# Optimization experiments

Hardware: AMD Instinct MI355X
Metric: run time of the kernel (lower is better)

The kernel has to match this reference:

```python
import jax, jax.numpy as jnp
import numpy as np

DIM = 1024
HEADS = 16
HEAD_DIM = DIM // HEADS
N_CLUSTERS = 8
B, N = 4, 1024


def setup_inputs() -> dict:
    key = jax.random.key(0)
    ks = jax.random.split(key, 10)
    s = 0.02
    return {
        "x": jax.random.normal(ks[0], (B, N, DIM), dtype=jnp.float32),
        "Wqkv": jax.random.normal(ks[1], (DIM, 3 * DIM), dtype=jnp.float32) * s,
        "Wproj": jax.random.normal(ks[2], (DIM, DIM), dtype=jnp.float32) * s,
        "bproj": jnp.zeros((DIM,), dtype=jnp.float32),
        "Wgroup": jax.random.normal(ks[3], (HEAD_DIM, N_CLUSTERS), dtype=jnp.float32) * s,
        "bgroup": jnp.zeros((N_CLUSTERS,), dtype=jnp.float32),
        "Wtheta": jax.random.normal(ks[4], (HEAD_DIM, 1), dtype=jnp.float32) * s,
        "btheta": jnp.zeros((1,), dtype=jnp.float32),
        "affinity_B": jax.random.normal(ks[5], (HEADS, N_CLUSTERS, N_CLUSTERS), dtype=jnp.float32),
        "cp_bias_scale": jnp.asarray(1.0, dtype=jnp.float32),
        "flag": 1,
        "injection": 0,
        "cp_dcmm": 1,
    }


def reference(x, Wqkv, Wproj, bproj, Wgroup, bgroup, Wtheta, btheta,
              affinity_B, cp_bias_scale, flag, injection, cp_dcmm):
    b, n, c = x.shape
    h = affinity_B.shape[0]
    hd = c // h
    scale = hd ** -0.5
    # qkv: [b,n,3c] -> [3,b,h,n,hd]
    qkv = (x @ Wqkv).reshape(b, n, 3, h, hd).transpose(2, 0, 3, 1, 4)
    q, k, v = qkv[0], qkv[1], qkv[2]
    attn = jnp.einsum('bhnd,bhmd->bhnm', q, k) * scale
    z_constraint = jnp.asarray(0.0, dtype=x.dtype)
    if cp_dcmm and flag:
        # cluster assignments per query token
        z = jax.nn.softmax(q @ Wgroup + bgroup, axis=-1)          # [b,h,n,K]
        B_aff = jax.nn.sigmoid(affinity_B)                         # [h,K,K]
        zB = jnp.einsum('bhik,hkl->bhil', z, B_aff)
        cp_bias_ori = jnp.tanh(jnp.einsum('bhil,bhjl->bhij', zB, z))  # [b,h,n,n]
        theta = jax.nn.relu(jnp.squeeze(q @ Wtheta + btheta, -1))  # [b,h,n]
        degree_term = theta[..., :, None] * theta[..., None, :]
        cp_bias = cp_bias_scale * degree_term * cp_bias_ori
        attn = attn + cp_bias
        z_constraint = -(z * jnp.log(z + 1e-8)).sum(axis=-1).mean()
    else:
        cp_bias = jnp.zeros_like(attn)
    attn = jax.nn.softmax(attn, axis=-1)
    out = jnp.einsum('bhnm,bhmd->bhnd', attn, v).transpose(0, 2, 1, 3).reshape(b, n, c)
    out = out @ Wproj + bproj
    zero = jnp.asarray(0.0, dtype=x.dtype)
    return (out, z_constraint, zero, zero, cp_bias)
```

## Files before the change

kernel.cpp:

```cpp
#include <hip/hip_runtime.h>
#include <stdint.h>

#define DIM 1024
#define HEADS 16
#define HD 64
#define NC 8
#define BB 4
#define NN 1024
#define ROWS (BB*NN)
#define TOK (BB*HEADS*NN)
#define OUT_OFF_Z (ROWS*DIM)
#define CP_OFF    (ROWS*DIM+3)

typedef __bf16 bf16_t;
typedef __attribute__((ext_vector_type(8))) __bf16 bf16x8;
typedef __attribute__((ext_vector_type(4))) __bf16 bf16x4;
typedef __attribute__((ext_vector_type(4))) float f32x4;

__device__ __forceinline__ void gload16(const void* g, void* l){
#if __has_builtin(__builtin_amdgcn_global_load_lds)
  __builtin_amdgcn_global_load_lds(
      (__attribute__((address_space(1))) void*)(g),
      (__attribute__((address_space(3))) void*)(l), 16, 0, 0);
#else
  *(uint4*)l = *(const uint4*)g;
#endif
}

__device__ __forceinline__ float tanh_poly(float d){
  float t2 = d*d;
  float p = -0.33333333f + t2*(0.13333333f + t2*(-0.05396825f));
  return d*(1.f + t2*p);
}

__global__ __launch_bounds__(256) void prep_kernel(
    const float* __restrict__ x, const float* __restrict__ Wqkv,
    const float* __restrict__ Wproj, const float* __restrict__ affB,
    bf16_t* __restrict__ xb, bf16_t* __restrict__ WqkvT, bf16_t* __restrict__ WprojT,
    float* __restrict__ sigB, float* __restrict__ out_scalars){
  const int bid = blockIdx.x, tid = threadIdx.x;
  if(bid < 4096){
    int i = (bid*256 + tid)*4;
    float4 v = *(const float4*)&x[i];
    bf16x4 o = {(bf16_t)v.x, (bf16_t)v.y, (bf16_t)v.z, (bf16_t)v.w};
    *(bf16x4*)&xb[i] = o;
    return;
  }
  if(bid < 8192){
    __shared__ float tile[32][33];
    const float* in; bf16_t* out; int K, N, bx, by;
    if(bid < 7168){ int t = bid-4096; in = Wqkv;  out = WqkvT;  K = 1024; N = 3072; bx = t%96; by = t/96; }
    else          { int t = bid-7168; in = Wproj; out = WprojT; K = 1024; N = 1024; bx = t%32; by = t/32; }
    int k0 = by*32, n0 = bx*32;
    int tx = tid & 31, ty = tid >> 5;
    #pragma unroll
    for(int r=ty; r<32; r+=8) tile[r][tx] = in[(size_t)(k0+r)*N + n0+tx];
    __syncthreads();
    #pragma unroll
    for(int r=ty; r<32; r+=8) out[(size_t)(n0+r)*K + k0+tx] = (bf16_t)tile[tx][r];
    return;
  }
  #pragma unroll
  for(int r=0;r<4;r++){
    int i = r*256 + tid;
    sigB[i] = 1.f/(1.f + __expf(-affB[i]));
  }
  if(tid < 3) out_scalars[tid] = 0.f;
}

__global__ __launch_bounds__(256) void gemm_qkvt(const bf16_t* __restrict__ xb,
                                                 const bf16_t* __restrict__ WT,
                                                 bf16_t* __restrict__ Qb,
                                                 bf16_t* __restrict__ Kb,
                                                 bf16_t* __restrict__ Vt){
  const int K = DIM;
  __shared__ __align__(16) bf16_t As[128*32];
  __shared__ __align__(16) bf16_t Bs[128*32];
  const int bid = blockIdx.x, tid = threadIdx.x;
  const bool qkmode = bid < 512;
  int m0, n0;
  const bf16_t *Ap, *Bp;
  if(qkmode){ m0 = (bid>>4)*128;            n0 = (bid&15)*128;
              Ap = xb + (size_t)m0*K;       Bp = WT + (size_t)n0*K; }
  else      { int t = bid-512; m0 = (t>>5)*128; n0 = (t&31)*128;
              Ap = WT + (size_t)(2048+m0)*K; Bp = xb + (size_t)n0*K; }
  const int wave = tid>>6, lane = tid&63, l15 = lane&15, quad = lane>>4;
  const int wm = (wave>>1)*64, wn = (wave&1)*64;

  f32x4 acc[4][4];
  #pragma unroll
  for(int i=0;i<4;i++)
    #pragma unroll
    for(int j=0;j<4;j++) acc[i][j] = (f32x4){0.f,0.f,0.f,0.f};

  for(int k0=0; k0<K; k0+=32){
    #pragma unroll
    for(int p=0;p<2;p++){
      int c = tid + p*256;
      int r = c>>2, s = c&3, xs = s ^ ((r>>1)&3);
      gload16(Ap + (size_t)r*K + k0 + xs*8, &As[c*8]);
      gload16(Bp + (size_t)r*K + k0 + xs*8, &Bs[c*8]);
    }
    __syncthreads();

    bf16x8 a[4], b[4];
    #pragma unroll
    for(int i=0;i<4;i++){
      int R = wm + i*16 + l15;
      a[i] = *(const bf16x8*)&As[R*32 + ((quad ^ ((R>>1)&3)))*8];
    }
    #pragma unroll
    for(int j=0;j<4;j++){
      int R = wn + j*16 + l15;
      b[j] = *(const bf16x8*)&Bs[R*32 + ((quad ^ ((R>>1)&3)))*8];
    }
    #pragma unroll
    for(int i=0;i<4;i++)
      #pragma unroll
      for(int j=0;j<4;j++)
        acc[i][j] = __builtin_amdgcn_mfma_f32_16x16x32_bf16(a[i], b[j], acc[i][j], 0,0,0);
    __syncthreads();
  }

  if(qkmode){
    #pragma unroll
    for(int j=0;j<4;j++){
      int col = n0 + wn + j*16 + l15;
      int which = col>>10, hc = col&1023, h = hc>>6, d = hc&63;
      bf16_t* dst = which ? Kb : Qb;
      #pragma unroll
      for(int i=0;i<4;i++){
        int m = m0 + wm + i*16 + quad*4;
        #pragma unroll
        for(int r=0;r<4;r++){
          int row = m + r;
          int bh = (row>>10)*HEADS + h, n = row&1023;
          dst[((size_t)bh*NN + n)*HD + d] = (bf16_t)acc[i][j][r];
        }
      }
    }
  } else {
    const int b = n0 >> 10;
    #pragma unroll
    for(int i=0;i<4;i++)
      #pragma unroll
      for(int j=0;j<4;j++){
        int vcol = m0 + wm + i*16 + quad*4;
        int ncol = (n0 & 1023) + wn + j*16 + l15;
        #pragma unroll
        for(int r=0;r<4;r++)
          Vt[((size_t)(b*1024 + vcol + r))*NN + ncol] = (bf16_t)acc[i][j][r];
      }
  }
}

__global__ __launch_bounds__(256) void token_kernel(
    const bf16_t* __restrict__ Qb, const float* __restrict__ Wgroup,
    const float* __restrict__ bgroup, const float* __restrict__ Wtheta,
    const float* __restrict__ btheta, const float* __restrict__ sigB,
    bf16_t* __restrict__ zb16, bf16_t* __restrict__ zBb16,
    float* __restrict__ thetaAll, float* __restrict__ entPart){
  const int wv = threadIdx.x>>6, lane = threadIdx.x&63;
  const int t = blockIdx.x*4 + wv;
  const int h = (t>>10)&15;
  float qd = (float)Qb[(size_t)t*HD + lane];

  float zl[8];
  #pragma unroll
  for(int c=0;c<8;c++){
    float p = qd * Wgroup[lane*NC + c];
    p += __shfl_xor(p,1);  p += __shfl_xor(p,2);  p += __shfl_xor(p,4);
    p += __shfl_xor(p,8);  p += __shfl_xor(p,16); p += __shfl_xor(p,32);
    zl[c] = p + bgroup[c];
  }
  float th = qd * Wtheta[lane];
  th += __shfl_xor(th,1);  th += __shfl_xor(th,2);  th += __shfl_xor(th,4);
  th += __shfl_xor(th,8);  th += __shfl_xor(th,16); th += __shfl_xor(th,32);
  th = fmaxf(th + btheta[0], 0.f);

  float mx = zl[0];
  #pragma unroll
  for(int c=1;c<8;c++) mx = fmaxf(mx, zl[c]);
  float ssum = 0.f;
  #pragma unroll
  for(int c=0;c<8;c++){ zl[c] = __expf(zl[c]-mx); ssum += zl[c]; }
  float inv = 1.f/ssum;
  float ent = 0.f;
  #pragma unroll
  for(int c=0;c<8;c++){ float z = zl[c]*inv; zl[c] = z; ent -= z*__logf(z + 1e-8f); }

  float zb[8];
  #pragma unroll
  for(int l=0;l<8;l++){
    float a = 0.f;
    #pragma unroll
    for(int k2=0;k2<8;k2++) a += zl[k2]*sigB[h*64 + k2*8 + l];
    zb[l] = a;
  }
  if(lane==0){
    bf16x8 zv, zbv;
    #pragma unroll
    for(int c=0;c<8;c++){ zv[c] = (bf16_t)zl[c]; zbv[c] = (bf16_t)zb[c]; }
    *(bf16x8*)&zb16[(size_t)t*8]  = zv;
    *(bf16x8*)&zBb16[(size_t)t*8] = zbv;
    thetaAll[t] = th;
  }

  __shared__ float es[4];
  if(lane==0) es[wv] = ent;
  __syncthreads();
  if(threadIdx.x==0) entPart[blockIdx.x] = es[0]+es[1]+es[2]+es[3];
}

__global__ __launch_bounds__(256) void bias_kernel(
    const bf16_t* __restrict__ zb16, const bf16_t* __restrict__ zBb16,
    const float* __restrict__ thetaAll, const float* __restrict__ cps_p,
    float* __restrict__ cp_out){
  const int bid = blockIdx.x;
  const int bh = bid & 63, qt = bid >> 6;
  const int tid = threadIdx.x;
  const int wave = tid>>6, lane = tid&63, l15 = lane&15, quad = lane>>4;
  __shared__ float thAll[NN];
  { float4 tv = *(const float4*)&thetaAll[(size_t)bh*NN + tid*4];
    *(float4*)&thAll[tid*4] = tv; }
  const float cps = cps_p[0];
  bf16x8 aZ = (bf16x8)(bf16_t)0.f;
  if(quad==0)
    aZ = *(const bf16x8*)&zBb16[((size_t)bh*NN + qt*64 + wave*16 + l15)*8];
  __syncthreads();
  float th_i[4];
  #pragma unroll
  for(int r=0;r<4;r++) th_i[r] = thAll[qt*64 + wave*16 + quad*4 + r];

  for(int kt=0; kt<16; ++kt){
    #pragma unroll
    for(int f=0;f<4;f++){
      bf16x8 bz = (bf16x8)(bf16_t)0.f;
      if(quad==0)
        bz = *(const bf16x8*)&zb16[((size_t)bh*NN + kt*64 + f*16 + l15)*8];
      f32x4 D = __builtin_amdgcn_mfma_f32_16x16x32_bf16(aZ, bz,
                  (f32x4){0.f,0.f,0.f,0.f}, 0,0,0);
      float thj = thAll[kt*64 + f*16 + l15];
      #pragma unroll
      for(int r=0;r<4;r++){
        float bv = cps * th_i[r] * thj * tanh_poly(D[r]);
        int irow = qt*64 + wave*16 + quad*4 + r;
        cp_out[((size_t)bh*NN + irow)*NN + (size_t)kt*64 + f*16 + l15] = bv;
      }
    }
  }
}

__global__ __launch_bounds__(256) void flash_kernel(
    const bf16_t* __restrict__ Qb, const bf16_t* __restrict__ Kb,
    const bf16_t* __restrict__ Vt, const bf16_t* __restrict__ zb16,
    const bf16_t* __restrict__ zBb16, const float* __restrict__ thetaAll,
    const float* __restrict__ cps_p, bf16_t* __restrict__ attnO){
  const int bid = blockIdx.x;
  const int bh = bid & 63, qt = bid >> 6;
  const int b = bh >> 4, h = bh & 15;
  const int tid = threadIdx.x;
  const int wave = tid>>6, lane = tid&63, l15 = lane&15, quad = lane>>4;

  __shared__ __align__(16) bf16_t Qs[128*64];
  __shared__ __align__(16) bf16_t Ks[64*64];
  __shared__ __align__(16) bf16_t Vs[64*64];
  __shared__ __align__(16) bf16_t Ps[4][16*72];
  __shared__ float thAll[NN];

  const float cps = cps_p[0];

  {
    const bf16_t* Qg = Qb + ((size_t)bh*NN + (size_t)qt*128)*HD;
    #pragma unroll
    for(int p=0;p<4;p++){
      int c = tid + p*256;
      int r = c>>3, xs = (c&7) ^ (r&7);
      gload16(Qg + r*64 + xs*8, &Qs[c*8]);
    }
    float4 tv = *(const float4*)&thetaAll[(size_t)bh*NN + tid*4];
    *(float4*)&thAll[tid*4] = tv;
  }
  bf16x8 aZ[2];
  #pragma unroll
  for(int qf=0;qf<2;qf++){
    aZ[qf] = (bf16x8)(bf16_t)0.f;
    if(quad==0)
      aZ[qf] = *(const bf16x8*)&zBb16[((size_t)bh*NN + qt*128 + wave*32 + qf*16 + l15)*8];
  }
  __syncthreads();

  float th_i[2][4];
  bf16x8 aq[2][2];
  #pragma unroll
  for(int qf=0;qf<2;qf++){
    int row = wave*32 + qf*16 + l15;
    aq[qf][0] = *(const bf16x8*)&Qs[row*64 + ((quad  ) ^ (row&7))*8];
    aq[qf][1] = *(const bf16x8*)&Qs[row*64 + ((quad+4) ^ (row&7))*8];
    #pragma unroll
    for(int r=0;r<4;r++)
      th_i[qf][r] = thAll[qt*128 + wave*32 + qf*16 + quad*4 + r];
  }

  float l_r[2][4] = {{0.f,0.f,0.f,0.f},{0.f,0.f,0.f,0.f}};
  f32x4 o[2][4];
  #pragma unroll
  for(int qf=0;qf<2;qf++)
    #pragma unroll
    for(int dn=0;dn<4;dn++) o[qf][dn] = (f32x4){0.f,0.f,0.f,0.f};

  for(int kt=0; kt<16; ++kt){
    const bf16_t* Kg = Kb + ((size_t)bh*NN + (size_t)kt*64)*HD;
    #pragma unroll
    for(int p=0;p<2;p++){
      int c = tid + p*256;
      int r = c>>3, xs = (c&7) ^ (r&7);
      gload16(Kg + r*64 + xs*8, &Ks[c*8]);
    }
    #pragma unroll
    for(int p=0;p<2;p++){
      int c = tid + p*256;
      int r = c>>3, xs = (c&7) ^ (r&7);
      gload16(Vt + (size_t)(bh*HD + r)*NN + kt*64 + xs*8, &Vs[c*8]);
    }

    float biasv[2][4][4];
    #pragma unroll
    for(int f=0;f<4;f++){
      bf16x8 bz = (bf16x8)(bf16_t)0.f;
      if(quad==0)
        bz = *(const bf16x8*)&zb16[((size_t)bh*NN + kt*64 + f*16 + l15)*8];
      float thj = thAll[kt*64 + f*16 + l15];
      #pragma unroll
      for(int qf=0;qf<2;qf++){
        f32x4 D = __builtin_amdgcn_mfma_f32_16x16x32_bf16(aZ[qf], bz,
                    (f32x4){0.f,0.f,0.f,0.f}, 0,0,0);
        #pragma unroll
        for(int r=0;r<4;r++)
          biasv[qf][f][r] = cps * th_i[qf][r] * thj * tanh_poly(D[r]);
      }
    }
    __syncthreads();

    #pragma unroll
    for(int qf=0;qf<2;qf++){
      f32x4 s[4];
      float rs[4] = {0.f,0.f,0.f,0.f};
      #pragma unroll
      for(int f=0;f<4;f++){
        int row = f*16 + l15;
        f32x4 z4 = (f32x4){0.f,0.f,0.f,0.f};
        bf16x8 b0 = *(const bf16x8*)&Ks[row*64 + ((quad  ) ^ (row&7))*8];
        bf16x8 b1 = *(const bf16x8*)&Ks[row*64 + ((quad+4) ^ (row&7))*8];
        z4 = __builtin_amdgcn_mfma_f32_16x16x32_bf16(aq[qf][0], b0, z4, 0,0,0);
        z4 = __builtin_amdgcn_mfma_f32_16x16x32_bf16(aq[qf][1], b1, z4, 0,0,0);
        #pragma unroll
        for(int r=0;r<4;r++){
          float p = __expf(z4[r]*0.125f + biasv[qf][f][r]);
          z4[r] = p;
          rs[r] += p;
        }
        s[f] = z4;
      }
      #pragma unroll
      for(int r=0;r<4;r++){
        float v = rs[r];
        v += __shfl_xor(v,1); v += __shfl_xor(v,2);
        v += __shfl_xor(v,4); v += __shfl_xor(v,8);
        l_r[qf][r] += v;
      }

      #pragma unroll
      for(int f=0;f<4;f++)
        #pragma unroll
        for(int r=0;r<4;r++)
          Ps[wave][(quad*4+r)*72 + f*16 + l15] = (bf16_t)s[f][r];

      bf16x8 pa0 = *(const bf16x8*)&Ps[wave][l15*72 + quad*8];
      bf16x8 pa1 = *(const bf16x8*)&Ps[wave][l15*72 + 32 + quad*8];
      #pragma unroll
      for(int dn=0;dn<4;dn++){
        int row = dn*16 + l15;
        bf16x8 b0 = *(const bf16x8*)&Vs[row*64 + ((quad  ) ^ (row&7))*8];
        bf16x8 b1 = *(const bf16x8*)&Vs[row*64 + ((quad+4) ^ (row&7))*8];
        o[qf][dn] = __builtin_amdgcn_mfma_f32_16x16x32_bf16(pa0, b0, o[qf][dn], 0,0,0);
        o[qf][dn] = __builtin_amdgcn_mfma_f32_16x16x32_bf16(pa1, b1, o[qf][dn], 0,0,0);
      }
    }
    __syncthreads();
  }

  #pragma unroll
  for(int qf=0;qf<2;qf++)
    #pragma unroll
    for(int r=0;r<4;r++){
      float inv = 1.f / l_r[qf][r];
      int grow = qt*128 + wave*32 + qf*16 + quad*4 + r;
      #pragma unroll
      for(int dn=0;dn<4;dn++)
        attnO[((size_t)(b*NN + grow))*DIM + h*HD + dn*16 + l15] = (bf16_t)(o[qf][dn][r]*inv);
    }
}

__global__ __launch_bounds__(256) void gemm_proj_ent(const bf16_t* __restrict__ A,
                                                     const bf16_t* __restrict__ Bt,
                                                     float* __restrict__ C,
                                                     const float* __restrict__ bias,
                                                     const float* __restrict__ entPart,
                                                     float* __restrict__ outz){
  const int bid = blockIdx.x, tid = threadIdx.x;
  if(bid == 512){
    float s = 0.f;
    for(int i=tid; i<TOK/4; i+=256) s += entPart[i];
    s += __shfl_xor(s,1); s += __shfl_xor(s,2); s += __shfl_xor(s,4);
    s += __shfl_xor(s,8); s += __shfl_xor(s,16); s += __shfl_xor(s,32);
    __shared__ float ls[4];
    if((tid&63)==0) ls[tid>>6] = s;
    __syncthreads();
    if(tid==0) outz[0] = (ls[0]+ls[1]+ls[2]+ls[3]) * (1.0f/(float)TOK);
    return;
  }
  const int K = DIM, N = DIM;
  __shared__ __align__(16) bf16_t As[128*32];
  __shared__ __align__(16) bf16_t Bs[64*32];
  const int m0 = (bid>>4)*128, n0 = (bid&15)*64;
  const int wave = tid>>6, lane = tid&63, l15 = lane&15, quad = lane>>4;
  const int wm = (wave>>1)*64, wn = (wave&1)*32;

  f32x4 acc[4][2];
  #pragma unroll
  for(int i=0;i<4;i++)
    #pragma unroll
    for(int j=0;j<2;j++) acc[i][j] = (f32x4){0.f,0.f,0.f,0.f};

  for(int k0=0; k0<K; k0+=32){
    {
      int c = tid;
      int r = c>>2, s = c&3, xs = s ^ ((r>>1)&3);
      gload16(A  + (size_t)(m0 + r)*K + k0 + xs*8, &As[c*8]);
      gload16(Bt + (size_t)(n0 + r)*K + k0 + xs*8, &Bs[c*8]);
      c = tid + 256;
      r = c>>2; s = c&3; xs = s ^ ((r>>1)&3);
      gload16(A  + (size_t)(m0 + r)*K + k0 + xs*8, &As[c*8]);
    }
    __syncthreads();

    bf16x8 a[4], b[2];
    #pragma unroll
    for(int i=0;i<4;i++){
      int R = wm + i*16 + l15;
      a[i] = *(const bf16x8*)&As[R*32 + ((quad ^ ((R>>1)&3)))*8];
    }
    #pragma unroll
    for(int j=0;j<2;j++){
      int R = wn + j*16 + l15;
      b[j] = *(const bf16x8*)&Bs[R*32 + ((quad ^ ((R>>1)&3)))*8];
    }
    #pragma unroll
    for(int i=0;i<4;i++)
      #pragma unroll
      for(int j=0;j<2;j++)
        acc[i][j] = __builtin_amdgcn_mfma_f32_16x16x32_bf16(a[i], b[j], acc[i][j], 0,0,0);
    __syncthreads();
  }

  #pragma unroll
  for(int i=0;i<4;i++)
    #pragma unroll
    for(int j=0;j<2;j++){
      int row = m0 + wm + i*16 + quad*4;
      int col = n0 + wn + j*16 + l15;
      float bv = bias[col];
      #pragma unroll
      for(int r=0;r<4;r++)
        C[(size_t)(row+r)*N + col] = acc[i][j][r] + bv;
    }
}

extern "C" void kernel_launch(void* const* d_in, const int* in_sizes, int n_in,
                              void* d_out, int out_size, void* d_ws, size_t ws_size,
                              hipStream_t stream){
  const float* x      = (const float*)d_in[0];
  const float* Wqkv   = (const float*)d_in[1];
  const float* Wproj  = (const float*)d_in[2];
  const float* bproj  = (const float*)d_in[3];
  const float* Wgroup = (const float*)d_in[4];
  const float* bgroup = (const float*)d_in[5];
  const float* Wtheta = (const float*)d_in[6];
  const float* btheta = (const float*)d_in[7];
  const float* affB   = (const float*)d_in[8];
  const float* cps    = (const float*)d_in[9];
  float* out = (float*)d_out;
  char* ws = (char*)d_ws;

  bf16_t* xb       = (bf16_t*)(ws);
  bf16_t* WqkvT    = (bf16_t*)(ws + (size_t)8*1048576);
  bf16_t* WprojT   = (bf16_t*)(ws + (size_t)14*1048576);
  bf16_t* Qb       = (bf16_t*)(ws + (size_t)16*1048576);
  bf16_t* Kb       = (bf16_t*)(ws + (size_t)24*1048576);
  bf16_t* Vt       = (bf16_t*)(ws + (size_t)32*1048576);
  bf16_t* zb16     = (bf16_t*)(ws + (size_t)40*1048576);
  bf16_t* zBb16    = (bf16_t*)(ws + (size_t)41*1048576);
  float*  thetaAll = (float*) (ws + (size_t)42*1048576);
  float*  entPart  = (float*) (ws + (size_t)43*1048576);
  bf16_t* attnO    = (bf16_t*)(ws + (size_t)44*1048576);
  float*  sigB     = (float*) (ws + (size_t)52*1048576);

  prep_kernel<<<8193, 256, 0, stream>>>(x, Wqkv, Wproj, affB, xb, WqkvT, WprojT,
                                        sigB, out + OUT_OFF_Z);
  gemm_qkvt<<<768, 256, 0, stream>>>(xb, WqkvT, Qb, Kb, Vt);
  token_kernel<<<TOK/4, 256, 0, stream>>>(Qb, Wgroup, bgroup, Wtheta, btheta, sigB,
                                          zb16, zBb16, thetaAll, entPart);
  bias_kernel<<<1024, 256, 0, stream>>>(zb16, zBb16, thetaAll, cps, out + CP_OFF);
  flash_kernel<<<512, 256, 0, stream>>>(Qb, Kb, Vt, zb16, zBb16, thetaAll,
                                        cps, attnO);
  gemm_proj_ent<<<513, 256, 0, stream>>>(attnO, WprojT, out, bproj,
                                         entPart, out + OUT_OFF_Z);
}
```

Measured before the change: 575.8 us.

## Use one thread per token in token kernel and merge bias writing into attention launch

The token kernel now gives each token its own thread instead of a whole wavefront. It stages the small weight matrices in shared memory and drops the per-element shuffle reductions, which shrinks the grid from 16384 blocks to 256. The separate cp_bias kernel becomes extra blocks in the attention kernel's grid, so the large bias writes can overlap with the flash-attention compute and one launch disappears. The entropy reduction is adjusted to the new block count. The bias blocks carry the flash kernel's large shared-memory allocation, which may limit how many of them are resident at once.

```diff
diff --git a/kernel.cpp b/kernel.cpp
--- a/kernel.cpp
+++ b/kernel.cpp
@@ -160,23 +160,40 @@
     const float* __restrict__ btheta, const float* __restrict__ sigB,
     bf16_t* __restrict__ zb16, bf16_t* __restrict__ zBb16,
     float* __restrict__ thetaAll, float* __restrict__ entPart){
-  const int wv = threadIdx.x>>6, lane = threadIdx.x&63;
-  const int t = blockIdx.x*4 + wv;
+  const int bid = blockIdx.x, tid = threadIdx.x;
+  const int t = bid*256 + tid;
   const int h = (t>>10)&15;
-  float qd = (float)Qb[(size_t)t*HD + lane];
-
-  float zl[8];
-  #pragma unroll
-  for(int c=0;c<8;c++){
-    float p = qd * Wgroup[lane*NC + c];
-    p += __shfl_xor(p,1);  p += __shfl_xor(p,2);  p += __shfl_xor(p,4);
-    p += __shfl_xor(p,8);  p += __shfl_xor(p,16); p += __shfl_xor(p,32);
-    zl[c] = p + bgroup[c];
-  }
-  float th = qd * Wtheta[lane];
-  th += __shfl_xor(th,1);  th += __shfl_xor(th,2);  th += __shfl_xor(th,4);
-  th += __shfl_xor(th,8);  th += __shfl_xor(th,16); th += __shfl_xor(th,32);
+  __shared__ float Wg[64][NC];
+  __shared__ float Wt[64];
+  __shared__ float sB[64];
+  __shared__ float bg[NC];
+  if(tid < 64){
+    #pragma unroll
+    for(int c=0;c<NC;c++) Wg[tid][c] = Wgroup[tid*NC + c];
+    Wt[tid] = Wtheta[tid];
+    sB[tid] = sigB[h*64 + tid];
+  }
+  if(tid < NC) bg[tid] = bgroup[tid];
+  __syncthreads();
+
+  float zl[8] = {0,0,0,0,0,0,0,0};
+  float th = 0.f;
+  const bf16_t* qrow = Qb + (size_t)t*HD;
+  #pragma unroll
+  for(int v=0; v<8; v++){
+    bf16x8 qv = *(const bf16x8*)&qrow[v*8];
+    #pragma unroll
+    for(int e=0;e<8;e++){
+      float qd = (float)qv[e];
+      int d = v*8+e;
+      #pragma unroll
+      for(int c=0;c<8;c++) zl[c] += qd * Wg[d][c];
+      th += qd * Wt[d];
+    }
+  }
   th = fmaxf(th + btheta[0], 0.f);
+  #pragma unroll
+  for(int c=0;c<8;c++) zl[c] += bg[c];
 
   float mx = zl[0];
   #pragma unroll
@@ -194,73 +211,34 @@
   for(int l=0;l<8;l++){
     float a = 0.f;
     #pragma unroll
-    for(int k2=0;k2<8;k2++) a += zl[k2]*sigB[h*64 + k2*8 + l];
+    for(int k2=0;k2<8;k2++) a += zl[k2]*sB[k2*8 + l];
     zb[l] = a;
   }
-  if(lane==0){
-    bf16x8 zv, zbv;
-    #pragma unroll
-    for(int c=0;c<8;c++){ zv[c] = (bf16_t)zl[c]; zbv[c] = (bf16_t)zb[c]; }
-    *(bf16x8*)&zb16[(size_t)t*8]  = zv;
-    *(bf16x8*)&zBb16[(size_t)t*8] = zbv;
-    thetaAll[t] = th;
-  }
-
+  bf16x8 zv, zbv;
+  #pragma unroll
+  for(int c=0;c<8;c++){ zv[c] = (bf16_t)zl[c]; zbv[c] = (bf16_t)zb[c]; }
+  *(bf16x8*)&zb16[(size_t)t*8]  = zv;
+  *(bf16x8*)&zBb16[(size_t)t*8] = zbv;
+  thetaAll[t] = th;
+
+  ent += __shfl_xor(ent,1);  ent += __shfl_xor(ent,2);  ent += __shfl_xor(ent,4);
+  ent += __shfl_xor(ent,8);  ent += __shfl_xor(ent,16); ent += __shfl_xor(ent,32);
   __shared__ float es[4];
-  if(lane==0) es[wv] = ent;
+  if((tid&63)==0) es[tid>>6] = ent;
   __syncthreads();
-  if(threadIdx.x==0) entPart[blockIdx.x] = es[0]+es[1]+es[2]+es[3];
-}
-
-__global__ __launch_bounds__(256) void bias_kernel(
-    const bf16_t* __restrict__ zb16, const bf16_t* __restrict__ zBb16,
-    const float* __restrict__ thetaAll, const float* __restrict__ cps_p,
-    float* __restrict__ cp_out){
-  const int bid = blockIdx.x;
-  const int bh = bid & 63, qt = bid >> 6;
-  const int tid = threadIdx.x;
-  const int wave = tid>>6, lane = tid&63, l15 = lane&15, quad = lane>>4;
-  __shared__ float thAll[NN];
-  { float4 tv = *(const float4*)&thetaAll[(size_t)bh*NN + tid*4];
-    *(float4*)&thAll[tid*4] = tv; }
-  const float cps = cps_p[0];
-  bf16x8 aZ = (bf16x8)(bf16_t)0.f;
-  if(quad==0)
-    aZ = *(const bf16x8*)&zBb16[((size_t)bh*NN + qt*64 + wave*16 + l15)*8];
-  __syncthreads();
-  float th_i[4];
-  #pragma unroll
-  for(int r=0;r<4;r++) th_i[r] = thAll[qt*64 + wave*16 + quad*4 + r];
-
-  for(int kt=0; kt<16; ++kt){
-    #pragma unroll
-    for(int f=0;f<4;f++){
-      bf16x8 bz = (bf16x8)(bf16_t)0.f;
-      if(quad==0)
-        bz = *(const bf16x8*)&zb16[((size_t)bh*NN + kt*64 + f*16 + l15)*8];
-      f32x4 D = __builtin_amdgcn_mfma_f32_16x16x32_bf16(aZ, bz,
-                  (f32x4){0.f,0.f,0.f,0.f}, 0,0,0);
-      float thj = thAll[kt*64 + f*16 + l15];
-      #pragma unroll
-      for(int r=0;r<4;r++){
-        float bv = cps * th_i[r] * thj * tanh_poly(D[r]);
-        int irow = qt*64 + wave*16 + quad*4 + r;
-        cp_out[((size_t)bh*NN + irow)*NN + (size_t)kt*64 + f*16 + l15] = bv;
-      }
-    }
-  }
-}
-
-__global__ __launch_bounds__(256) void flash_kernel(
+  if(tid==0) entPart[bid] = es[0]+es[1]+es[2]+es[3];
+}
+
+__global__ __launch_bounds__(256) void attn_kernel(
     const bf16_t* __restrict__ Qb, const bf16_t* __restrict__ Kb,
     const bf16_t* __restrict__ Vt, const bf16_t* __restrict__ zb16,
     const bf16_t* __restrict__ zBb16, const float* __restrict__ thetaAll,
-    const float* __restrict__ cps_p, bf16_t* __restrict__ attnO){
+    const float* __restrict__ cps_p, float* __restrict__ cp_out,
+    bf16_t* __restrict__ attnO){
   const int bid = blockIdx.x;
-  const int bh = bid & 63, qt = bid >> 6;
-  const int b = bh >> 4, h = bh & 15;
   const int tid = threadIdx.x;
   const int wave = tid>>6, lane = tid&63, l15 = lane&15, quad = lane>>4;
+  const float cps = cps_p[0];
 
   __shared__ __align__(16) bf16_t Qs[128*64];
   __shared__ __align__(16) bf16_t Ks[64*64];
@@ -268,7 +246,41 @@
   __shared__ __align__(16) bf16_t Ps[4][16*72];
   __shared__ float thAll[NN];
 
-  const float cps = cps_p[0];
+  if(bid >= 512){
+    const int b2 = bid - 512;
+    const int bh = b2 & 63, qt = b2 >> 6;
+    { float4 tv = *(const float4*)&thetaAll[(size_t)bh*NN + tid*4];
+      *(float4*)&thAll[tid*4] = tv; }
+    bf16x8 aZ = (bf16x8)(bf16_t)0.f;
+    if(quad==0)
+      aZ = *(const bf16x8*)&zBb16[((size_t)bh*NN + qt*64 + wave*16 + l15)*8];
+    __syncthreads();
+    float th_i[4];
+    #pragma unroll
+    for(int r=0;r<4;r++) th_i[r] = thAll[qt*64 + wave*16 + quad*4 + r];
+
+    for(int kt=0; kt<16; ++kt){
+      #pragma unroll
+      for(int f=0;f<4;f++){
+        bf16x8 bz = (bf16x8)(bf16_t)0.f;
+        if(quad==0)
+          bz = *(const bf16x8*)&zb16[((size_t)bh*NN + kt*64 + f*16 + l15)*8];
+        f32x4 D = __builtin_amdgcn_mfma_f32_16x16x32_bf16(aZ, bz,
+                    (f32x4){0.f,0.f,0.f,0.f}, 0,0,0);
+        float thj = thAll[kt*64 + f*16 + l15];
+        #pragma unroll
+        for(int r=0;r<4;r++){
+          float bv = cps * th_i[r] * thj * tanh_poly(D[r]);
+          int irow = qt*64 + wave*16 + quad*4 + r;
+          cp_out[((size_t)bh*NN + irow)*NN + (size_t)kt*64 + f*16 + l15] = bv;
+        }
+      }
+    }
+    return;
+  }
+
+  const int bh = bid & 63, qt = bid >> 6;
+  const int b = bh >> 4, h = bh & 15;
 
   {
     const bf16_t* Qg = Qb + ((size_t)bh*NN + (size_t)qt*128)*HD;
@@ -410,8 +422,7 @@
                                                      float* __restrict__ outz){
   const int bid = blockIdx.x, tid = threadIdx.x;
   if(bid == 512){
-    float s = 0.f;
-    for(int i=tid; i<TOK/4; i+=256) s += entPart[i];
+    float s = (tid < 256) ? entPart[tid] : 0.f;
     s += __shfl_xor(s,1); s += __shfl_xor(s,2); s += __shfl_xor(s,4);
     s += __shfl_xor(s,8); s += __shfl_xor(s,16); s += __shfl_xor(s,32);
     __shared__ float ls[4];
@@ -509,11 +520,10 @@
   prep_kernel<<<8193, 256, 0, stream>>>(x, Wqkv, Wproj, affB, xb, WqkvT, WprojT,
                                         sigB, out + OUT_OFF_Z);
   gemm_qkvt<<<768, 256, 0, stream>>>(xb, WqkvT, Qb, Kb, Vt);
-  token_kernel<<<TOK/4, 256, 0, stream>>>(Qb, Wgroup, bgroup, Wtheta, btheta, sigB,
-                                          zb16, zBb16, thetaAll, entPart);
-  bias_kernel<<<1024, 256, 0, stream>>>(zb16, zBb16, thetaAll, cps, out + CP_OFF);
-  flash_kernel<<<512, 256, 0, stream>>>(Qb, Kb, Vt, zb16, zBb16, thetaAll,
-                                        cps, attnO);
+  token_kernel<<<256, 256, 0, stream>>>(Qb, Wgroup, bgroup, Wtheta, btheta, sigB,
+                                        zb16, zBb16, thetaAll, entPart);
+  attn_kernel<<<1536, 256, 0, stream>>>(Qb, Kb, Vt, zb16, zBb16, thetaAll,
+                                        cps, out + CP_OFF, attnO);
   gemm_proj_ent<<<513, 256, 0, stream>>>(attnO, WprojT, out, bproj,
                                          entPart, out + OUT_OFF_Z);
 }
```

Result: faster. 478.5 us (-16.9%).
